# Kernel tuning notes

Measured on AMD Instinct MI355X. Metric: run time of the kernel, lower is better.

## Reference

```python
import jax, jax.numpy as jnp
import numpy as np

GAMMA = 1.5
BN_EPS = 1e-5


def sparsemax(z):
    """Sparsemax along last axis (Martins & Astudillo, 2016)."""
    z = z - jnp.max(z, axis=-1, keepdims=True)
    z_sorted = -jnp.sort(-z, axis=-1)                      # descending sort
    z_cumsum = jnp.cumsum(z_sorted, axis=-1)
    k = jnp.arange(1, z.shape[-1] + 1, dtype=z.dtype)
    support = (z_sorted - (z_cumsum - 1.0) / k) > 0
    k_z = jnp.clip(jnp.sum(support, axis=-1, keepdims=True), 1, None).astype(z.dtype)
    idx = (k_z - 1.0).astype(jnp.int32)
    tau = (jnp.take_along_axis(z_cumsum, idx, axis=-1) - 1.0) / k_z
    return jnp.clip(z - tau, 0.0, None)


def setup_inputs() -> dict:
    key = jax.random.key(0)
    k1, k2 = jax.random.split(key)
    B, T, E, H = 32, 512, 512, 8
    x = jax.random.normal(k1, (B, T, E), dtype=jnp.float32)
    # torch Linear weight (out, in), kaiming-ish scale
    W = jax.random.normal(k2, (H, E, E), dtype=jnp.float32) / np.float32(np.sqrt(E))
    bn_weight = jnp.ones((H, E), dtype=jnp.float32)
    bn_bias = jnp.zeros((H, E), dtype=jnp.float32)
    return {"x": x, "W": W, "bn_weight": bn_weight, "bn_bias": bn_bias}


def reference(x, W, bn_weight, bn_bias):
    B, T, E = x.shape
    H = W.shape[0]
    gi = x.reshape(B * T, E)
    # all-head linear: y[n,o] = sum_i gi[n,i] * W[h,o,i]
    logits = jnp.einsum('ni,hoi->hno', gi, W)              # (H, B*T, E)
    # BatchNorm1d in training mode: batch stats over the B*T axis, biased var
    mean = jnp.mean(logits, axis=1, keepdims=True)
    var = jnp.var(logits, axis=1, keepdims=True)
    logits = (logits - mean) / jnp.sqrt(var + BN_EPS)
    logits = logits * bn_weight[:, None, :] + bn_bias[:, None, :]
    logits = logits.reshape(H, B, T, E)

    prior0 = jnp.ones((B, T, E), dtype=x.dtype)

    def step(prior, logits_h):
        mask_h = sparsemax(logits_h * prior)
        prior = prior * jnp.clip(GAMMA - mask_h, 0.0, None)
        return prior, mask_h

    _, masks = jax.lax.scan(step, prior0, logits)          # masks: (H, B, T, E)
    masked_xs = x[None, :, :, :] * masks                   # (H, B, T, E)
    return masked_xs, jnp.transpose(masks, (1, 0, 2, 3))   # (B, H, T, E)
```

## Files before the change

kernel.cpp:

```cpp
#include <hip/hip_runtime.h>
#include <stdint.h>

#define Hh 8
#define Bb 32
#define Tt 512
#define Ee 512
#define Nn 16384
#define GAMMA_ 1.5f
#define BN_EPS_ 1e-5f

typedef _Float16 f16x4 __attribute__((ext_vector_type(4)));
typedef _Float16 f16x8 __attribute__((ext_vector_type(8)));
typedef float    f32x4 __attribute__((ext_vector_type(4)));

__device__ __forceinline__ void async_ld16(void* lds, const void* g) {
    __builtin_amdgcn_global_load_lds(
        (const __attribute__((address_space(1))) void*)g,
        (__attribute__((address_space(3))) void*)lds, 16, 0, 0);
}

__device__ __forceinline__ float dpp_sum64(float v) {
    int t;
    t = __builtin_amdgcn_update_dpp(0, __float_as_int(v), 0x111, 0xf, 0xf, true);
    v += __int_as_float(t);
    t = __builtin_amdgcn_update_dpp(0, __float_as_int(v), 0x112, 0xf, 0xf, true);
    v += __int_as_float(t);
    t = __builtin_amdgcn_update_dpp(0, __float_as_int(v), 0x114, 0xf, 0xf, true);
    v += __int_as_float(t);
    t = __builtin_amdgcn_update_dpp(0, __float_as_int(v), 0x118, 0xf, 0xf, true);
    v += __int_as_float(t);
    t = __builtin_amdgcn_update_dpp(0, __float_as_int(v), 0x142, 0xf, 0xf, true);
    v += __int_as_float(t);
    t = __builtin_amdgcn_update_dpp(0, __float_as_int(v), 0x143, 0xf, 0xf, true);
    v += __int_as_float(t);
    return __int_as_float(__builtin_amdgcn_readlane(__float_as_int(v), 63));
}

__global__ __launch_bounds__(256) void cvt_kernel(const float* __restrict__ x,
                                                  const float* __restrict__ W,
                                                  _Float16* __restrict__ xh,
                                                  _Float16* __restrict__ wh) {
    const int NX = Bb * Tt * Ee;
    int i = (blockIdx.x * 256 + threadIdx.x) * 4;
    if (i < NX) {
        float4 v = *(const float4*)(x + i);
        f16x4 o = {(_Float16)v.x, (_Float16)v.y, (_Float16)v.z, (_Float16)v.w};
        *(f16x4*)(xh + i) = o;
    } else {
        int j = i - NX;
        float4 v = *(const float4*)(W + j);
        f16x4 o = {(_Float16)v.x, (_Float16)v.y, (_Float16)v.z, (_Float16)v.w};
        *(f16x4*)(wh + j) = o;
    }
}

__global__ __launch_bounds__(256) void gemm_kernel(const _Float16* __restrict__ A,
                                                   const _Float16* __restrict__ Bm,
                                                   _Float16* __restrict__ C,
                                                   float* __restrict__ sums,
                                                   float* __restrict__ sumsq) {
    __shared__ alignas(16) _Float16 As[2][128 * 32];
    __shared__ alignas(16) _Float16 Bs[2][128 * 32];
    const int h  = blockIdx.z;
    const int mb = blockIdx.x * 128;
    const int nb = blockIdx.y * 128;
    const int t    = threadIdx.x;
    const int lane = t & 63;
    const int w    = t >> 6;
    const int wm   = (w >> 1) * 64;
    const int wn   = (w & 1) * 64;
    const int quad = lane >> 4;
    const int l16  = lane & 15;

    const _Float16* Ap = A + (size_t)(mb + (t >> 2)) * Ee + (t & 3) * 8;
    const _Float16* Bp = Bm + (size_t)h * Ee * Ee + (size_t)(nb + (t >> 2)) * Ee + (t & 3) * 8;

    f32x4 acc[4][4] = {};

    async_ld16(&As[0][t * 8],        Ap);
    async_ld16(&As[0][2048 + t * 8], Ap + 64 * Ee);
    async_ld16(&Bs[0][t * 8],        Bp);
    async_ld16(&Bs[0][2048 + t * 8], Bp + 64 * Ee);

    int buf = 0;
    for (int k0 = 0; k0 < Ee; k0 += 32) {
        __syncthreads();
        if (k0 + 32 < Ee) {
            int nb2 = buf ^ 1;
            async_ld16(&As[nb2][t * 8],        Ap + k0 + 32);
            async_ld16(&As[nb2][2048 + t * 8], Ap + 64 * Ee + k0 + 32);
            async_ld16(&Bs[nb2][t * 8],        Bp + k0 + 32);
            async_ld16(&Bs[nb2][2048 + t * 8], Bp + 64 * Ee + k0 + 32);
        }
        f16x8 a8[4], b8[4];
#pragma unroll
        for (int mt = 0; mt < 4; ++mt)
            a8[mt] = *(const f16x8*)(&As[buf][(wm + mt * 16 + l16) * 32 + quad * 8]);
#pragma unroll
        for (int nt = 0; nt < 4; ++nt)
            b8[nt] = *(const f16x8*)(&Bs[buf][(wn + nt * 16 + l16) * 32 + quad * 8]);
#pragma unroll
        for (int mt = 0; mt < 4; ++mt)
#pragma unroll
            for (int nt = 0; nt < 4; ++nt)
                acc[mt][nt] = __builtin_amdgcn_mfma_f32_16x16x32_f16(a8[mt], b8[nt], acc[mt][nt], 0, 0, 0);
        buf ^= 1;
    }

#pragma unroll
    for (int nt = 0; nt < 4; ++nt) {
        float s = 0.f, ss = 0.f;
#pragma unroll
        for (int mt = 0; mt < 4; ++mt)
#pragma unroll
            for (int r = 0; r < 4; ++r) { float v = acc[mt][nt][r]; s += v; ss += v * v; }
        s  += __shfl_xor(s, 16, 64);  s  += __shfl_xor(s, 32, 64);
        ss += __shfl_xor(ss, 16, 64); ss += __shfl_xor(ss, 32, 64);
        if (quad == 0) {
            int col = nb + wn + nt * 16 + l16;
            atomicAdd(&sums[h * Ee + col], s);
            atomicAdd(&sumsq[h * Ee + col], ss);
        }
    }

    _Float16* Cp = C + (size_t)h * Nn * Ee;
#pragma unroll
    for (int mt = 0; mt < 4; ++mt)
#pragma unroll
        for (int r = 0; r < 4; ++r) {
            int row = mb + wm + mt * 16 + quad * 4 + r;
            size_t off = (size_t)row * Ee + nb + wn + l16;
#pragma unroll
            for (int nt = 0; nt < 4; ++nt)
                Cp[off + nt * 16] = (_Float16)acc[mt][nt][r];
        }
}

__global__ __launch_bounds__(256) void stats_kernel(const float* __restrict__ sums,
                                                    const float* __restrict__ sumsq,
                                                    const float* __restrict__ bnw,
                                                    const float* __restrict__ bnb,
                                                    float* __restrict__ cA,
                                                    float* __restrict__ cB) {
    int i = blockIdx.x * 256 + threadIdx.x;
    float mean = sums[i] * (1.0f / Nn);
    float var  = sumsq[i] * (1.0f / Nn) - mean * mean;
    float inv  = rsqrtf(var + BN_EPS_);
    float a    = bnw[i] * inv;
    cA[i] = a;
    cB[i] = bnb[i] - mean * a;
}

__global__ __launch_bounds__(256) void rows_kernel(const float* __restrict__ x,
                                                   const _Float16* __restrict__ lg,
                                                   const float* __restrict__ cA,
                                                   const float* __restrict__ cB,
                                                   float* __restrict__ out) {
    const int n    = blockIdx.x * 4 + (threadIdx.x >> 6);
    const int lane = threadIdx.x & 63;
    const int e0   = lane * 4;
    const int bb   = n >> 9;
    const int tt   = n & 511;

    float xr[8], prior[8], z[8], mk[8];
    {
        const float* xp = x + (size_t)n * Ee;
        float4 x0 = *(const float4*)(xp + e0);
        float4 x1 = *(const float4*)(xp + 256 + e0);
        xr[0]=x0.x; xr[1]=x0.y; xr[2]=x0.z; xr[3]=x0.w;
        xr[4]=x1.x; xr[5]=x1.y; xr[6]=x1.z; xr[7]=x1.w;
    }
#pragma unroll
    for (int j = 0; j < 8; ++j) prior[j] = 1.0f;

    float* omx = out;
    float* omk = out + (size_t)Hh * Nn * Ee;

    const _Float16* lp0 = lg + (size_t)n * Ee;
    f16x4 l0 = *(const f16x4*)(lp0 + e0);
    f16x4 l1 = *(const f16x4*)(lp0 + 256 + e0);

#pragma unroll
    for (int h = 0; h < Hh; ++h) {
        f16x4 n0, n1;
        if (h + 1 < Hh) {
            const _Float16* lpn = lg + (size_t)(h + 1) * Nn * Ee + (size_t)n * Ee;
            n0 = *(const f16x4*)(lpn + e0);
            n1 = *(const f16x4*)(lpn + 256 + e0);
        }
        const float* ap = cA + h * Ee;
        const float* bp = cB + h * Ee;
        float4 a0 = *(const float4*)(ap + e0);
        float4 a1 = *(const float4*)(ap + 256 + e0);
        float4 b0 = *(const float4*)(bp + e0);
        float4 b1 = *(const float4*)(bp + 256 + e0);
        float av[8] = {a0.x,a0.y,a0.z,a0.w,a1.x,a1.y,a1.z,a1.w};
        float bv[8] = {b0.x,b0.y,b0.z,b0.w,b1.x,b1.y,b1.z,b1.w};
        float lv[8] = {(float)l0[0],(float)l0[1],(float)l0[2],(float)l0[3],
                       (float)l1[0],(float)l1[1],(float)l1[2],(float)l1[3]};
#pragma unroll
        for (int j = 0; j < 8; ++j)
            z[j] = (lv[j] * av[j] + bv[j]) * prior[j];

        float sl = 0.f;
#pragma unroll
        for (int j = 0; j < 8; ++j) sl += z[j];
        float tau = (dpp_sum64(sl) - 1.0f) * (1.0f / 512.0f);
        int cprev = 512;
        for (int it = 0; it < 64; ++it) {
            float s2 = 0.f, cf = 0.f;
#pragma unroll
            for (int j = 0; j < 8; ++j) {
                bool p = z[j] > tau;
                s2 += p ? z[j] : 0.0f;
                cf += p ? 1.0f : 0.0f;
            }
            float S = dpp_sum64(s2);
            float Cc = dpp_sum64(cf);
            int c = (int)Cc;
            if (c == cprev) break;
            cprev = c;
            tau = (S - 1.0f) / Cc;
        }

#pragma unroll
        for (int j = 0; j < 8; ++j) {
            mk[j] = fmaxf(z[j] - tau, 0.0f);
            prior[j] *= fmaxf(GAMMA_ - mk[j], 0.0f);
        }

        size_t oxoff = ((size_t)h * Nn + n) * Ee;
        size_t okoff = (((size_t)bb * Hh + h) * Tt + tt) * Ee;
        f32x4 vx0 = {xr[0]*mk[0], xr[1]*mk[1], xr[2]*mk[2], xr[3]*mk[3]};
        f32x4 vx1 = {xr[4]*mk[4], xr[5]*mk[5], xr[6]*mk[6], xr[7]*mk[7]};
        f32x4 vm0 = {mk[0], mk[1], mk[2], mk[3]};
        f32x4 vm1 = {mk[4], mk[5], mk[6], mk[7]};
        __builtin_nontemporal_store(vx0, (f32x4*)(omx + oxoff + e0));
        __builtin_nontemporal_store(vx1, (f32x4*)(omx + oxoff + 256 + e0));
        __builtin_nontemporal_store(vm0, (f32x4*)(omk + okoff + e0));
        __builtin_nontemporal_store(vm1, (f32x4*)(omk + okoff + 256 + e0));
        l0 = n0; l1 = n1;
    }
}

extern "C" void kernel_launch(void* const* d_in, const int* in_sizes, int n_in,
                              void* d_out, int out_size, void* d_ws, size_t ws_size,
                              hipStream_t stream) {
    const float* x   = (const float*)d_in[0];
    const float* W   = (const float*)d_in[1];
    const float* bnw = (const float*)d_in[2];
    const float* bnb = (const float*)d_in[3];
    float* out = (float*)d_out;

    uint8_t* ws = (uint8_t*)d_ws;
    _Float16* xh = (_Float16*)(ws);
    _Float16* wh = (_Float16*)(ws + 16777216);
    _Float16* lg = (_Float16*)(ws + 20971520);
    float* sums  = (float*)(ws + 155189248);
    float* sumsq = (float*)(ws + 155205632);
    float* cA    = (float*)(ws + 155222016);
    float* cB    = (float*)(ws + 155238400);

    hipMemsetAsync(sums, 0, 2 * 4096 * sizeof(float), stream);

    cvt_kernel<<<10240, 256, 0, stream>>>(x, W, xh, wh);
    gemm_kernel<<<dim3(128, 4, 8), 256, 0, stream>>>(xh, wh, lg, sums, sumsq);
    stats_kernel<<<16, 256, 0, stream>>>(sums, sumsq, bnw, bnb, cA, cB);
    rows_kernel<<<4096, 256, 0, stream>>>(x, lg, cA, cB, out);
}
```

Before: 676.0 us.

## Swizzle GEMM block order for L2 reuse and keep rows loop rolled

```diff
diff --git a/kernel.cpp b/kernel.cpp
--- a/kernel.cpp
+++ b/kernel.cpp
@@ -61,9 +61,15 @@
                                                    float* __restrict__ sumsq) {
     __shared__ alignas(16) _Float16 As[2][128 * 32];
     __shared__ alignas(16) _Float16 Bs[2][128 * 32];
-    const int h  = blockIdx.z;
-    const int mb = blockIdx.x * 128;
-    const int nb = blockIdx.y * 128;
+    const int id = blockIdx.x;
+    const int g  = id >> 5;
+    const int r  = id & 31;
+    const int h  = g >> 4;
+    const int q  = r & 7;
+    const int s  = r >> 3;
+    const int mb = ((g & 15) * 8 + (q & 3) * 2 + (s & 1)) * 128;
+    const int nb = ((q >> 2) * 2 + (s >> 1)) * 128;
+
     const int t    = threadIdx.x;
     const int lane = t & 63;
     const int w    = t >> 6;
@@ -109,16 +115,16 @@
 
 #pragma unroll
     for (int nt = 0; nt < 4; ++nt) {
-        float s = 0.f, ss = 0.f;
+        float sv = 0.f, ss = 0.f;
 #pragma unroll
         for (int mt = 0; mt < 4; ++mt)
 #pragma unroll
-            for (int r = 0; r < 4; ++r) { float v = acc[mt][nt][r]; s += v; ss += v * v; }
-        s  += __shfl_xor(s, 16, 64);  s  += __shfl_xor(s, 32, 64);
+            for (int rr = 0; rr < 4; ++rr) { float v = acc[mt][nt][rr]; sv += v; ss += v * v; }
+        sv += __shfl_xor(sv, 16, 64); sv += __shfl_xor(sv, 32, 64);
         ss += __shfl_xor(ss, 16, 64); ss += __shfl_xor(ss, 32, 64);
         if (quad == 0) {
             int col = nb + wn + nt * 16 + l16;
-            atomicAdd(&sums[h * Ee + col], s);
+            atomicAdd(&sums[h * Ee + col], sv);
             atomicAdd(&sumsq[h * Ee + col], ss);
         }
     }
@@ -127,12 +133,12 @@
 #pragma unroll
     for (int mt = 0; mt < 4; ++mt)
 #pragma unroll
-        for (int r = 0; r < 4; ++r) {
-            int row = mb + wm + mt * 16 + quad * 4 + r;
+        for (int rr = 0; rr < 4; ++rr) {
+            int row = mb + wm + mt * 16 + quad * 4 + rr;
             size_t off = (size_t)row * Ee + nb + wn + l16;
 #pragma unroll
             for (int nt = 0; nt < 4; ++nt)
-                Cp[off + nt * 16] = (_Float16)acc[mt][nt][r];
+                Cp[off + nt * 16] = (_Float16)acc[mt][nt][rr];
         }
 }
 
@@ -162,7 +168,7 @@
     const int bb   = n >> 9;
     const int tt   = n & 511;
 
-    float xr[8], prior[8], z[8], mk[8];
+    float xr[8], prior[8];
     {
         const float* xp = x + (size_t)n * Ee;
         float4 x0 = *(const float4*)(xp + e0);
@@ -176,37 +182,42 @@
     float* omx = out;
     float* omk = out + (size_t)Hh * Nn * Ee;
 
-    const _Float16* lp0 = lg + (size_t)n * Ee;
-    f16x4 l0 = *(const f16x4*)(lp0 + e0);
-    f16x4 l1 = *(const f16x4*)(lp0 + 256 + e0);
-
-#pragma unroll
+    const _Float16* lrow = lg + (size_t)n * Ee;
+    f16x4 l0 = *(const f16x4*)(lrow + e0);
+    f16x4 l1 = *(const f16x4*)(lrow + 256 + e0);
+
+#pragma unroll 1
     for (int h = 0; h < Hh; ++h) {
-        f16x4 n0, n1;
+        f16x4 p0 = l0, p1 = l1;
         if (h + 1 < Hh) {
-            const _Float16* lpn = lg + (size_t)(h + 1) * Nn * Ee + (size_t)n * Ee;
-            n0 = *(const f16x4*)(lpn + e0);
-            n1 = *(const f16x4*)(lpn + 256 + e0);
-        }
-        const float* ap = cA + h * Ee;
-        const float* bp = cB + h * Ee;
-        float4 a0 = *(const float4*)(ap + e0);
-        float4 a1 = *(const float4*)(ap + 256 + e0);
-        float4 b0 = *(const float4*)(bp + e0);
-        float4 b1 = *(const float4*)(bp + 256 + e0);
-        float av[8] = {a0.x,a0.y,a0.z,a0.w,a1.x,a1.y,a1.z,a1.w};
-        float bv[8] = {b0.x,b0.y,b0.z,b0.w,b1.x,b1.y,b1.z,b1.w};
-        float lv[8] = {(float)l0[0],(float)l0[1],(float)l0[2],(float)l0[3],
-                       (float)l1[0],(float)l1[1],(float)l1[2],(float)l1[3]};
-#pragma unroll
-        for (int j = 0; j < 8; ++j)
-            z[j] = (lv[j] * av[j] + bv[j]) * prior[j];
+            const _Float16* lnx = lrow + (size_t)(h + 1) * Nn * Ee;
+            p0 = *(const f16x4*)(lnx + e0);
+            p1 = *(const f16x4*)(lnx + 256 + e0);
+        }
+        float z[8];
+        {
+            const float* ap = cA + h * Ee + e0;
+            const float* bp = cB + h * Ee + e0;
+            float4 a0 = *(const float4*)(ap);
+            float4 b0 = *(const float4*)(bp);
+            float4 a1 = *(const float4*)(ap + 256);
+            float4 b1 = *(const float4*)(bp + 256);
+            z[0] = ((float)l0[0] * a0.x + b0.x) * prior[0];
+            z[1] = ((float)l0[1] * a0.y + b0.y) * prior[1];
+            z[2] = ((float)l0[2] * a0.z + b0.z) * prior[2];
+            z[3] = ((float)l0[3] * a0.w + b0.w) * prior[3];
+            z[4] = ((float)l1[0] * a1.x + b1.x) * prior[4];
+            z[5] = ((float)l1[1] * a1.y + b1.y) * prior[5];
+            z[6] = ((float)l1[2] * a1.z + b1.z) * prior[6];
+            z[7] = ((float)l1[3] * a1.w + b1.w) * prior[7];
+        }
 
         float sl = 0.f;
 #pragma unroll
         for (int j = 0; j < 8; ++j) sl += z[j];
         float tau = (dpp_sum64(sl) - 1.0f) * (1.0f / 512.0f);
         int cprev = 512;
+#pragma unroll 1
         for (int it = 0; it < 64; ++it) {
             float s2 = 0.f, cf = 0.f;
 #pragma unroll
@@ -215,7 +226,7 @@
                 s2 += p ? z[j] : 0.0f;
                 cf += p ? 1.0f : 0.0f;
             }
-            float S = dpp_sum64(s2);
+            float S  = dpp_sum64(s2);
             float Cc = dpp_sum64(cf);
             int c = (int)Cc;
             if (c == cprev) break;
@@ -223,23 +234,26 @@
             tau = (S - 1.0f) / Cc;
         }
 
-#pragma unroll
-        for (int j = 0; j < 8; ++j) {
-            mk[j] = fmaxf(z[j] - tau, 0.0f);
-            prior[j] *= fmaxf(GAMMA_ - mk[j], 0.0f);
-        }
-
-        size_t oxoff = ((size_t)h * Nn + n) * Ee;
-        size_t okoff = (((size_t)bb * Hh + h) * Tt + tt) * Ee;
-        f32x4 vx0 = {xr[0]*mk[0], xr[1]*mk[1], xr[2]*mk[2], xr[3]*mk[3]};
-        f32x4 vx1 = {xr[4]*mk[4], xr[5]*mk[5], xr[6]*mk[6], xr[7]*mk[7]};
-        f32x4 vm0 = {mk[0], mk[1], mk[2], mk[3]};
-        f32x4 vm1 = {mk[4], mk[5], mk[6], mk[7]};
-        __builtin_nontemporal_store(vx0, (f32x4*)(omx + oxoff + e0));
-        __builtin_nontemporal_store(vx1, (f32x4*)(omx + oxoff + 256 + e0));
-        __builtin_nontemporal_store(vm0, (f32x4*)(omk + okoff + e0));
-        __builtin_nontemporal_store(vm1, (f32x4*)(omk + okoff + 256 + e0));
-        l0 = n0; l1 = n1;
+        size_t oxoff = ((size_t)h * Nn + n) * Ee + e0;
+        size_t okoff = (((size_t)bb * Hh + h) * Tt + tt) * Ee + e0;
+        f32x4 vx, vm;
+#pragma unroll
+        for (int j = 0; j < 4; ++j) {
+            float m = fmaxf(z[j] - tau, 0.0f);
+            prior[j] *= fmaxf(GAMMA_ - m, 0.0f);
+            vm[j] = m; vx[j] = xr[j] * m;
+        }
+        __builtin_nontemporal_store(vx, (f32x4*)(omx + oxoff));
+        __builtin_nontemporal_store(vm, (f32x4*)(omk + okoff));
+#pragma unroll
+        for (int j = 0; j < 4; ++j) {
+            float m = fmaxf(z[4 + j] - tau, 0.0f);
+            prior[4 + j] *= fmaxf(GAMMA_ - m, 0.0f);
+            vm[j] = m; vx[j] = xr[4 + j] * m;
+        }
+        __builtin_nontemporal_store(vx, (f32x4*)(omx + oxoff + 256));
+        __builtin_nontemporal_store(vm, (f32x4*)(omk + okoff + 256));
+        l0 = p0; l1 = p1;
     }
 }
 
@@ -264,7 +278,7 @@
     hipMemsetAsync(sums, 0, 2 * 4096 * sizeof(float), stream);
 
     cvt_kernel<<<10240, 256, 0, stream>>>(x, W, xh, wh);
-    gemm_kernel<<<dim3(128, 4, 8), 256, 0, stream>>>(xh, wh, lg, sums, sumsq);
+    gemm_kernel<<<4096, 256, 0, stream>>>(xh, wh, lg, sums, sumsq);
     stats_kernel<<<16, 256, 0, stream>>>(sums, sumsq, bnw, bnb, cA, cB);
     rows_kernel<<<4096, 256, 0, stream>>>(x, lg, cA, cB, out);
 }
```

After: 698.1 us. 1.03x slower.
